# Kernel tuning notes

Hardware: AMD Instinct MI355X
Metric: run time of the kernel (lower is better)

## Reference

```python
import jax, jax.numpy as jnp
import numpy as np

B, T, E = 8, 2048, 2048

def setup_inputs() -> dict:
    key = jax.random.key(0)
    k1, k2, k3 = jax.random.split(key, 3)
    x = jax.random.normal(k1, (B, T, E), dtype=jnp.float32)
    weight = jax.random.normal(k2, (T,), dtype=jnp.float32)
    bias = jax.random.normal(k3, (T,), dtype=jnp.float32)
    return {"x": x, "weight": weight, "bias": bias}

def _toeplitz_matrix(v, T):
    # M[i, j] = v[j - i] for j >= i, else 0  (upper-triangular Toeplitz)
    idx = jnp.arange(T)
    diff = idx[None, :] - idx[:, None]          # [T, T], diff = j - i
    M = jnp.where(diff >= 0, v[jnp.clip(diff, 0, T - 1)], jnp.zeros((), v.dtype))
    return M

def reference(x, weight, bias):
    Tlen = x.shape[1]
    W = _toeplitz_matrix(weight[:Tlen], Tlen).astype(x.dtype)  # [T, T]
    # original: out[b,e,t'] = sum_t x[b,e,t] * W[t,t']; in (B,T,E) layout:
    out = jnp.einsum('bte,ts->bse', x, W)
    out = out + bias[:Tlen][None, :, None]
    return out
```

## Files before the change

kernel.cpp:

```cpp
#include <hip/hip_runtime.h>
#include <hip/hip_bf16.h>

#define T_LEN 2048
#define E_LEN 2048
#define B_SZ  8
#define BM 256
#define BN 256
#define BK2 64
#define WREV_LEN 4104
#define CL 2312
#define ABUF_B 32768
#define BOFF (3 * ABUF_B)

typedef short short8 __attribute__((ext_vector_type(8)));
typedef float floatx4 __attribute__((ext_vector_type(4)));

typedef const __attribute__((address_space(1))) void* gas_ptr;
typedef __attribute__((address_space(3))) void* lds_ptr;

__global__ __launch_bounds__(256) void transpose_cast(
    const float* __restrict__ x, __hip_bfloat16* __restrict__ xT)
{
    const int t0 = blockIdx.x * 64, e0 = blockIdx.y * 64, b = blockIdx.z;
    __shared__ unsigned int W[64][33];
    const int tid = threadIdx.x;
    const int wave = tid >> 6, lane = tid & 63;

    const float* xb = x + (size_t)b * T_LEN * E_LEN;
    const int c = tid & 15;
    const int q = tid >> 4;

    #pragma unroll
    for (int i = 0; i < 2; ++i) {
        const int tp = q + 16 * i;
        const float4 a4 = *reinterpret_cast<const float4*>(
            xb + (size_t)(t0 + 2 * tp) * E_LEN + e0 + 4 * c);
        const float4 b4 = *reinterpret_cast<const float4*>(
            xb + (size_t)(t0 + 2 * tp + 1) * E_LEN + e0 + 4 * c);
        const float av[4] = {a4.x, a4.y, a4.z, a4.w};
        const float bv[4] = {b4.x, b4.y, b4.z, b4.w};
        #pragma unroll
        for (int j = 0; j < 4; ++j) {
            __hip_bfloat16 ha = __float2bfloat16(av[j]);
            __hip_bfloat16 hb = __float2bfloat16(bv[j]);
            unsigned int w =
                (unsigned int)*reinterpret_cast<unsigned short*>(&ha) |
                ((unsigned int)*reinterpret_cast<unsigned short*>(&hb) << 16);
            W[4 * c + j][tp] = w;
        }
    }
    __syncthreads();

    __hip_bfloat16* xTb = xT + (size_t)b * E_LEN * T_LEN;
    const int er = lane >> 3;
    const int pc = (lane & 7) * 4;
    #pragma unroll
    for (int i = 0; i < 2; ++i) {
        const int e = wave * 8 + i * 32 + er;
        uint4 v;
        v.x = W[e][pc + 0];
        v.y = W[e][pc + 1];
        v.z = W[e][pc + 2];
        v.w = W[e][pc + 3];
        unsigned int* dst =
            reinterpret_cast<unsigned int*>(xTb + (size_t)(e0 + e) * T_LEN + t0);
        *reinterpret_cast<uint4*>(dst + pc) = v;
    }
}

__global__ __launch_bounds__(256) void build_wrevs(
    const float* __restrict__ w, __hip_bfloat16* __restrict__ wrevs)
{
    int total = 8 * WREV_LEN;
    for (int i = threadIdx.x + blockIdx.x * blockDim.x; i < total;
         i += blockDim.x * gridDim.x) {
        int p = i / WREV_LEN, q = i - p * WREV_LEN;
        int j = q + p;
        float v = (j < T_LEN) ? w[T_LEN - 1 - j] : 0.0f;
        wrevs[i] = __float2bfloat16(v);
    }
}

#define LOAD_A8(dst, KK)                                                       \
    _Pragma("unroll")                                                          \
    for (int mi = 0; mi < 8; ++mi) {                                           \
        const int r = wm + mi * 16 + ln15;                                     \
        const int xq = ((KK) * 4 + quad) ^ (ln15 & 7);                         \
        dst[mi] = *reinterpret_cast<const short8*>(Ab + r * 128 + xq * 16);    \
    }

#define LOAD_B4(dst, KK)                                                       \
    _Pragma("unroll")                                                          \
    for (int ni = 0; ni < 4; ++ni) {                                           \
        const int C = Cb + t0 + (KK) * 32 - ni * 16;                           \
        const int p = C & 7;                                                   \
        dst[ni] = *reinterpret_cast<const short8*>(                            \
            L + BOFF + p * (CL * 2) + ((C - p) - Wbase) * 2);                  \
    }

#define MFMA32(Af, Bf)                                                         \
    _Pragma("unroll")                                                          \
    for (int ni = 0; ni < 4; ++ni)                                             \
        _Pragma("unroll")                                                      \
        for (int mi = 0; mi < 8; ++mi)                                         \
            acc[mi][ni] = __builtin_amdgcn_mfma_f32_16x16x32_bf16(             \
                Af[mi], Bf[ni], acc[mi][ni], 0, 0, 0);

__global__ __launch_bounds__(512, 2) void toeplitz_gemm(
    const __hip_bfloat16* __restrict__ xT,
    const __hip_bfloat16* __restrict__ wrevs,
    const float* __restrict__ bias,
    float* __restrict__ out)
{
    __shared__ __align__(16) char L[3 * ABUF_B + 8 * CL * 2];

    const int bid = blockIdx.x;
    const int xcd = bid & 7, r5 = bid >> 3;
    const int panel = xcd * 8 + (r5 & 7);
    const int pi = r5 >> 3;
    const int mb = panel & 7, b = panel >> 3;
    const int e0 = mb * BM;
    const int tid = threadIdx.x;
    const int wave = tid >> 6, lane = tid & 63;
    const int wm = (wave >> 2) * 128;
    const int wn = (wave & 3) * 64;
    const int ln15 = lane & 15, quad = lane >> 4;

    const __hip_bfloat16* xTb = xT + ((size_t)b * E_LEN + e0) * T_LEN;

    auto STAGE1 = [&](int buf, int kt2, int cc) {
        const int t0n = kt2 * BK2;
        const int c = cc * 512 + tid;
        const int rr = c >> 3, p = c & 7;
        const int ps = p ^ (rr & 7);
        const __hip_bfloat16* g = xTb + (size_t)rr * T_LEN + t0n + ps * 8;
        __builtin_amdgcn_global_load_lds(
            (gas_ptr)g,
            (lds_ptr)(L + buf * ABUF_B + (cc * 512 + wave * 64) * 16), 16, 0, 0);
    };

    for (int run = 0; run < 2; ++run) {
        const int nb = (run == 0) ? 7 - pi : pi;
        const int s0 = nb * BN;
        const int ktiles = 4 * (nb + 1);
        const int Wbase = T_LEN - 264 - s0;
        const int Cb = (T_LEN - 1 - s0 - wn - ln15) + quad * 8;

        __syncthreads();
        for (int i = tid; i < 8 * (CL / 8); i += 512) {
            const int p = i / (CL / 8), c = i - p * (CL / 8);
            int q = Wbase + c * 8;
            if (q < 0) q = 0;
            const uint4 v = *(reinterpret_cast<const uint4*>(
                wrevs + (size_t)p * WREV_LEN + q));
            *(reinterpret_cast<uint4*>(L + BOFF + (size_t)p * (CL * 2)) + c) = v;
        }

        floatx4 acc[8][4];
        #pragma unroll
        for (int i = 0; i < 8; ++i)
            #pragma unroll
            for (int j = 0; j < 4; ++j)
                acc[i][j] = (floatx4){0.f, 0.f, 0.f, 0.f};

        STAGE1(0, 0, 0); STAGE1(0, 0, 1); STAGE1(0, 0, 2); STAGE1(0, 0, 3);
        STAGE1(1, 1, 0); STAGE1(1, 1, 1); STAGE1(1, 1, 2); STAGE1(1, 1, 3);
        asm volatile("s_waitcnt vmcnt(4) lgkmcnt(0)" ::: "memory");
        __builtin_amdgcn_s_barrier();

        int bi = 0;
        for (int kt = 0; kt < ktiles; ++kt) {
            const int t0 = kt * BK2;
            const char* Ab = L + bi * ABUF_B;
            const bool pf = (kt + 2 < ktiles);
            const int bp = (bi + 2 >= 3) ? bi - 1 : bi + 2;

            if (pf) {
                STAGE1(bp, kt + 2, 0); STAGE1(bp, kt + 2, 1);
                STAGE1(bp, kt + 2, 2); STAGE1(bp, kt + 2, 3);
            }

            short8 afr0[8], bfr0[4], afr1[8], bfr1[4];
            LOAD_A8(afr0, 0)
            LOAD_B4(bfr0, 0)
            LOAD_A8(afr1, 1)

            __builtin_amdgcn_s_setprio(1);
            MFMA32(afr0, bfr0)
            __builtin_amdgcn_s_setprio(0);

            LOAD_B4(bfr1, 1)

            __builtin_amdgcn_s_setprio(1);
            MFMA32(afr1, bfr1)
            __builtin_amdgcn_s_setprio(0);

            if (pf) asm volatile("s_waitcnt vmcnt(4)" ::: "memory");
            else    asm volatile("s_waitcnt vmcnt(0)" ::: "memory");
            __builtin_amdgcn_s_barrier();

            bi = (bi + 1 == 3) ? 0 : bi + 1;
        }

        #pragma unroll
        for (int ni = 0; ni < 4; ++ni) {
            const int s = s0 + wn + ni * 16 + ln15;
            const float bv = bias[s];
            #pragma unroll
            for (int mi = 0; mi < 8; ++mi) {
                const int e = e0 + wm + mi * 16 + quad * 4;
                float* dst = out + ((size_t)b * T_LEN + s) * E_LEN + e;
                floatx4 v = acc[mi][ni];
                v.x += bv; v.y += bv; v.z += bv; v.w += bv;
                *reinterpret_cast<floatx4*>(dst) = v;
            }
        }
    }
}

extern "C" void kernel_launch(void* const* d_in, const int* in_sizes, int n_in,
                              void* d_out, int out_size, void* d_ws, size_t ws_size,
                              hipStream_t stream)
{
    const float* x    = (const float*)d_in[0];
    const float* w    = (const float*)d_in[1];
    const float* bias = (const float*)d_in[2];
    float* out = (float*)d_out;

    __hip_bfloat16* xT = (__hip_bfloat16*)d_ws;
    __hip_bfloat16* wrevs =
        (__hip_bfloat16*)((char*)d_ws + (size_t)B_SZ * E_LEN * T_LEN * 2);

    transpose_cast<<<dim3(T_LEN / 64, E_LEN / 64, B_SZ), 256, 0, stream>>>(x, xT);
    build_wrevs<<<dim3(64), 256, 0, stream>>>(w, wrevs);
    toeplitz_gemm<<<dim3(256), 512, 0, stream>>>(xT, wrevs, bias, out);
}
```

Measured before the change: 298.9 us.

## Fuse fp32-to-bf16 transpose into GEMM with register-staged double buffering

Removes the separate transpose_cast kernel and its bf16 workspace round trip. The GEMM now reads fp32 x directly into registers, converts and packs pairs to bf16, and writes them transposed into a double-buffered, XOR-swizzled LDS tile. The triple-buffered async global_load_lds pipeline becomes a two-buffer register-staged one. This saves a full read and write of x through HBM, but adds conversion ALU work and register pressure inside the GEMM and reads each x tile once per N-block pass in fp32, so the kernel moves twice the bytes per tile.

Result: no change. 298.4 us (-0.2%).

```diff
diff --git a/kernel.cpp b/kernel.cpp
--- a/kernel.cpp
+++ b/kernel.cpp
@@ -10,63 +10,10 @@
 #define WREV_LEN 4104
 #define CL 2312
 #define ABUF_B 32768
-#define BOFF (3 * ABUF_B)
+#define BOFF (2 * ABUF_B)
 
 typedef short short8 __attribute__((ext_vector_type(8)));
 typedef float floatx4 __attribute__((ext_vector_type(4)));
-
-typedef const __attribute__((address_space(1))) void* gas_ptr;
-typedef __attribute__((address_space(3))) void* lds_ptr;
-
-__global__ __launch_bounds__(256) void transpose_cast(
-    const float* __restrict__ x, __hip_bfloat16* __restrict__ xT)
-{
-    const int t0 = blockIdx.x * 64, e0 = blockIdx.y * 64, b = blockIdx.z;
-    __shared__ unsigned int W[64][33];
-    const int tid = threadIdx.x;
-    const int wave = tid >> 6, lane = tid & 63;
-
-    const float* xb = x + (size_t)b * T_LEN * E_LEN;
-    const int c = tid & 15;
-    const int q = tid >> 4;
-
-    #pragma unroll
-    for (int i = 0; i < 2; ++i) {
-        const int tp = q + 16 * i;
-        const float4 a4 = *reinterpret_cast<const float4*>(
-            xb + (size_t)(t0 + 2 * tp) * E_LEN + e0 + 4 * c);
-        const float4 b4 = *reinterpret_cast<const float4*>(
-            xb + (size_t)(t0 + 2 * tp + 1) * E_LEN + e0 + 4 * c);
-        const float av[4] = {a4.x, a4.y, a4.z, a4.w};
-        const float bv[4] = {b4.x, b4.y, b4.z, b4.w};
-        #pragma unroll
-        for (int j = 0; j < 4; ++j) {
-            __hip_bfloat16 ha = __float2bfloat16(av[j]);
-            __hip_bfloat16 hb = __float2bfloat16(bv[j]);
-            unsigned int w =
-                (unsigned int)*reinterpret_cast<unsigned short*>(&ha) |
-                ((unsigned int)*reinterpret_cast<unsigned short*>(&hb) << 16);
-            W[4 * c + j][tp] = w;
-        }
-    }
-    __syncthreads();
-
-    __hip_bfloat16* xTb = xT + (size_t)b * E_LEN * T_LEN;
-    const int er = lane >> 3;
-    const int pc = (lane & 7) * 4;
-    #pragma unroll
-    for (int i = 0; i < 2; ++i) {
-        const int e = wave * 8 + i * 32 + er;
-        uint4 v;
-        v.x = W[e][pc + 0];
-        v.y = W[e][pc + 1];
-        v.z = W[e][pc + 2];
-        v.w = W[e][pc + 3];
-        unsigned int* dst =
-            reinterpret_cast<unsigned int*>(xTb + (size_t)(e0 + e) * T_LEN + t0);
-        *reinterpret_cast<uint4*>(dst + pc) = v;
-    }
-}
 
 __global__ __launch_bounds__(256) void build_wrevs(
     const float* __restrict__ w, __hip_bfloat16* __restrict__ wrevs)
@@ -85,7 +32,7 @@
     _Pragma("unroll")                                                          \
     for (int mi = 0; mi < 8; ++mi) {                                           \
         const int r = wm + mi * 16 + ln15;                                     \
-        const int xq = ((KK) * 4 + quad) ^ (ln15 & 7);                         \
+        const int xq = ((KK) * 4 + quad) ^ (r & 7) ^ ((r >> 3) & 7);           \
         dst[mi] = *reinterpret_cast<const short8*>(Ab + r * 128 + xq * 16);    \
     }
 
@@ -95,7 +42,7 @@
         const int C = Cb + t0 + (KK) * 32 - ni * 16;                           \
         const int p = C & 7;                                                   \
         dst[ni] = *reinterpret_cast<const short8*>(                            \
-            L + BOFF + p * (CL * 2) + ((C - p) - Wbase) * 2);                  \
+            Lsh + BOFF + p * (CL * 2) + ((C - p) - Wbase) * 2);                \
     }
 
 #define MFMA32(Af, Bf)                                                         \
@@ -106,13 +53,16 @@
             acc[mi][ni] = __builtin_amdgcn_mfma_f32_16x16x32_bf16(             \
                 Af[mi], Bf[ni], acc[mi][ni], 0, 0, 0);
 
+#define TILE_BARRIER()                                                         \
+    asm volatile("s_waitcnt lgkmcnt(0)\n\ts_barrier" ::: "memory");
+
 __global__ __launch_bounds__(512, 2) void toeplitz_gemm(
-    const __hip_bfloat16* __restrict__ xT,
+    const float* __restrict__ x,
     const __hip_bfloat16* __restrict__ wrevs,
     const float* __restrict__ bias,
     float* __restrict__ out)
 {
-    __shared__ __align__(16) char L[3 * ABUF_B + 8 * CL * 2];
+    __shared__ __align__(16) char Lsh[BOFF + 8 * CL * 2];
 
     const int bid = blockIdx.x;
     const int xcd = bid & 7, r5 = bid >> 3;
@@ -126,17 +76,37 @@
     const int wn = (wave & 3) * 64;
     const int ln15 = lane & 15, quad = lane >> 4;
 
-    const __hip_bfloat16* xTb = xT + ((size_t)b * E_LEN + e0) * T_LEN;
+    const float* xb = x + (size_t)b * T_LEN * E_LEN + e0;
 
-    auto STAGE1 = [&](int buf, int kt2, int cc) {
-        const int t0n = kt2 * BK2;
-        const int c = cc * 512 + tid;
-        const int rr = c >> 3, p = c & 7;
-        const int ps = p ^ (rr & 7);
-        const __hip_bfloat16* g = xTb + (size_t)rr * T_LEN + t0n + ps * 8;
-        __builtin_amdgcn_global_load_lds(
-            (gas_ptr)g,
-            (lds_ptr)(L + buf * ABUF_B + (cc * 512 + wave * 64) * 16), 16, 0, 0);
+    float4 La[8];
+    auto LOADX = [&](int kt2) {
+        const float* g = xb + (size_t)(kt2 * BK2 + 8 * wave) * E_LEN + 4 * lane;
+        #pragma unroll
+        for (int tt = 0; tt < 8; ++tt)
+            La[tt] = *reinterpret_cast<const float4*>(g + (size_t)tt * E_LEN);
+    };
+    auto PACKWRITE = [&](int buf) {
+        char* base = Lsh + buf * ABUF_B;
+        #pragma unroll
+        for (int j = 0; j < 4; ++j) {
+            const int r = 4 * lane + j;
+            const int s = wave ^ (r & 7) ^ ((r >> 3) & 7);
+            unsigned int tmp[4];
+            #pragma unroll
+            for (int k = 0; k < 4; ++k) {
+                const float fa[4] = {La[2 * k].x, La[2 * k].y,
+                                     La[2 * k].z, La[2 * k].w};
+                const float fb[4] = {La[2 * k + 1].x, La[2 * k + 1].y,
+                                     La[2 * k + 1].z, La[2 * k + 1].w};
+                __hip_bfloat16 ha = __float2bfloat16(fa[j]);
+                __hip_bfloat16 hb = __float2bfloat16(fb[j]);
+                tmp[k] =
+                    (unsigned int)*reinterpret_cast<unsigned short*>(&ha) |
+                    ((unsigned int)*reinterpret_cast<unsigned short*>(&hb) << 16);
+            }
+            uint4 wv = {tmp[0], tmp[1], tmp[2], tmp[3]};
+            *reinterpret_cast<uint4*>(base + r * 128 + s * 16) = wv;
+        }
     };
 
     for (int run = 0; run < 2; ++run) {
@@ -153,7 +123,7 @@
             if (q < 0) q = 0;
             const uint4 v = *(reinterpret_cast<const uint4*>(
                 wrevs + (size_t)p * WREV_LEN + q));
-            *(reinterpret_cast<uint4*>(L + BOFF + (size_t)p * (CL * 2)) + c) = v;
+            *(reinterpret_cast<uint4*>(Lsh + BOFF + (size_t)p * (CL * 2)) + c) = v;
         }
 
         floatx4 acc[8][4];
@@ -163,43 +133,34 @@
             for (int j = 0; j < 4; ++j)
                 acc[i][j] = (floatx4){0.f, 0.f, 0.f, 0.f};
 
-        STAGE1(0, 0, 0); STAGE1(0, 0, 1); STAGE1(0, 0, 2); STAGE1(0, 0, 3);
-        STAGE1(1, 1, 0); STAGE1(1, 1, 1); STAGE1(1, 1, 2); STAGE1(1, 1, 3);
-        asm volatile("s_waitcnt vmcnt(4) lgkmcnt(0)" ::: "memory");
-        __builtin_amdgcn_s_barrier();
+        LOADX(0);
+        PACKWRITE(0);
+        LOADX(1);
+        TILE_BARRIER();
 
-        int bi = 0;
+        int cur = 0;
         for (int kt = 0; kt < ktiles; ++kt) {
             const int t0 = kt * BK2;
-            const char* Ab = L + bi * ABUF_B;
-            const bool pf = (kt + 2 < ktiles);
-            const int bp = (bi + 2 >= 3) ? bi - 1 : bi + 2;
+            const char* Ab = Lsh + cur * ABUF_B;
 
-            if (pf) {
-                STAGE1(bp, kt + 2, 0); STAGE1(bp, kt + 2, 1);
-                STAGE1(bp, kt + 2, 2); STAGE1(bp, kt + 2, 3);
-            }
+            if (kt + 1 < ktiles) PACKWRITE(cur ^ 1);
+            if (kt + 2 < ktiles) LOADX(kt + 2);
 
-            short8 afr0[8], bfr0[4], afr1[8], bfr1[4];
-            LOAD_A8(afr0, 0)
-            LOAD_B4(bfr0, 0)
-            LOAD_A8(afr1, 1)
-
+            short8 afr[8], bfr[4];
+            LOAD_A8(afr, 0)
+            LOAD_B4(bfr, 0)
             __builtin_amdgcn_s_setprio(1);
-            MFMA32(afr0, bfr0)
+            MFMA32(afr, bfr)
             __builtin_amdgcn_s_setprio(0);
 
-            LOAD_B4(bfr1, 1)
-
+            LOAD_A8(afr, 1)
+            LOAD_B4(bfr, 1)
             __builtin_amdgcn_s_setprio(1);
-            MFMA32(afr1, bfr1)
+            MFMA32(afr, bfr)
             __builtin_amdgcn_s_setprio(0);
 
-            if (pf) asm volatile("s_waitcnt vmcnt(4)" ::: "memory");
-            else    asm volatile("s_waitcnt vmcnt(0)" ::: "memory");
-            __builtin_amdgcn_s_barrier();
-
-            bi = (bi + 1 == 3) ? 0 : bi + 1;
+            TILE_BARRIER();
+            cur ^= 1;
         }
 
         #pragma unroll
@@ -227,11 +188,8 @@
     const float* bias = (const float*)d_in[2];
     float* out = (float*)d_out;
 
-    __hip_bfloat16* xT = (__hip_bfloat16*)d_ws;
-    __hip_bfloat16* wrevs =
-        (__hip_bfloat16*)((char*)d_ws + (size_t)B_SZ * E_LEN * T_LEN * 2);
+    __hip_bfloat16* wrevs = (__hip_bfloat16*)d_ws;
 
-    transpose_cast<<<dim3(T_LEN / 64, E_LEN / 64, B_SZ), 256, 0, stream>>>(x, xT);
     build_wrevs<<<dim3(64), 256, 0, stream>>>(w, wrevs);
-    toeplitz_gemm<<<dim3(256), 512, 0, stream>>>(xT, wrevs, bias, out);
+    toeplitz_gemm<<<dim3(256), 512, 0, stream>>>(x, wrevs, bias, out);
 }
```
